# Kernel optimization log

Hardware: AMD Instinct MI355X
Metric: run time of the kernel (lower is better)

Reference implementation:

```python
import jax, jax.numpy as jnp
import numpy as np

H = 16          # num_attention_heads
D = 1024        # hidden_size
HD = D // H     # attention_head_size = 64


def setup_inputs() -> dict:
    key = jax.random.key(0)
    ks = jax.random.split(key, 9)
    s = 1.0 / np.sqrt(D)
    return {
        "hidden_states": jax.random.normal(ks[0], (4, 1024, D), jnp.float32),
        "encoder_hidden_states": jax.random.normal(ks[1], (4, 1024, D), jnp.float32),
        "attention_mask": jnp.zeros((4, 1, 1, 2048), jnp.float32),
        "Wq": jax.random.normal(ks[2], (D, D), jnp.float32) * s,
        "bq": jnp.zeros((D,), jnp.float32),
        "Wk": jax.random.normal(ks[3], (D, D), jnp.float32) * s,
        "bk": jnp.zeros((D,), jnp.float32),
        "Wv": jax.random.normal(ks[4], (D, D), jnp.float32) * s,
        "bv": jnp.zeros((D,), jnp.float32),
    }


def _split_heads(x):
    # [B, S, D] -> [B, H, S, HD]
    B, S, _ = x.shape
    return x.reshape(B, S, H, HD).transpose(0, 2, 1, 3)


def reference(hidden_states, encoder_hidden_states, attention_mask, Wq, bq, Wk, bk, Wv, bv):
    # KV over concat(encoder, decoder); Q over decoder hidden states only.
    all_hidden = jnp.concatenate([encoder_hidden_states, hidden_states], axis=1)  # [B, Skv, D]
    q = _split_heads(hidden_states @ Wq + bq)        # [B, H, Sq, HD]
    k = _split_heads(all_hidden @ Wk + bk)           # [B, H, Skv, HD]
    v = _split_heads(all_hidden @ Wv + bv)           # [B, H, Skv, HD]

    scores = jnp.einsum("bhqd,bhkd->bhqk", q, k) / np.sqrt(HD).astype(np.float32)
    scores = scores + attention_mask                 # additive mask, broadcast
    probs = jax.nn.softmax(scores, axis=-1)          # dropout p=0 (eval)
    ctx = jnp.einsum("bhqk,bhkd->bhqd", probs, v)    # [B, H, Sq, HD]
    B, _, Sq, _ = ctx.shape
    return ctx.transpose(0, 2, 1, 3).reshape(B, Sq, D)
```

## Files before the change

### kernel.cpp

```cpp
#include <hip/hip_runtime.h>


typedef _Float16 f16;
typedef __attribute__((ext_vector_type(4))) _Float16 half4;
typedef __attribute__((ext_vector_type(8))) _Float16 half8;
typedef __attribute__((ext_vector_type(4))) float floatx4;
typedef __attribute__((ext_vector_type(16))) float floatx16;
typedef __attribute__((ext_vector_type(4))) unsigned int uint4v;

__global__ void wt_kernel(const float* __restrict__ W, f16* __restrict__ Wt) {
    __shared__ float tile[32][33];
    int k0 = blockIdx.y * 32, n0 = blockIdx.x * 32;
    int tx = threadIdx.x, ty = threadIdx.y;
    #pragma unroll
    for (int i = 0; i < 32; i += 8)
        tile[ty + i][tx] = W[(k0 + ty + i) * 1024 + n0 + tx];
    __syncthreads();
    #pragma unroll
    for (int i = 0; i < 32; i += 8)
        Wt[(n0 + ty + i) * 1024 + k0 + tx] = (f16)tile[tx][ty + i];
}

__global__ void cvt_kernel(const float* __restrict__ hid, const float* __restrict__ enc,
                           f16* __restrict__ Aall) {
    int t = blockIdx.x * 256 + threadIdx.x;
    int rowg = t >> 7, col = (t & 127) * 8;
    int b = rowg >> 11, r = rowg & 2047;
    const float* src = (r < 1024 ? enc + ((size_t)b * 1024 + r) * 1024
                                 : hid + ((size_t)b * 1024 + (r - 1024)) * 1024) + col;
    float4 v0 = *(const float4*)src, v1 = *(const float4*)(src + 4);
    half8 o;
    o[0] = (f16)v0.x; o[1] = (f16)v0.y; o[2] = (f16)v0.z; o[3] = (f16)v0.w;
    o[4] = (f16)v1.x; o[5] = (f16)v1.y; o[6] = (f16)v1.z; o[7] = (f16)v1.w;
    *(half8*)(Aall + (size_t)rowg * 1024 + col) = o;
}

__launch_bounds__(256)
__global__ void qkv_gemm(const f16* __restrict__ Aall, const f16* __restrict__ Wt,
                         const float* __restrict__ bias, f16* __restrict__ out, int mode) {
    __shared__ f16 At[128 * 40];
    __shared__ f16 Bt[128 * 40];

    int tid = threadIdx.x;
    int m0 = blockIdx.x * 128, n0 = blockIdx.y * 128;
    int wid = tid >> 6, lane = tid & 63;
    int wm = (wid >> 1) * 64, wn = (wid & 1) * 64;
    int lr = lane & 15, lg = lane >> 4;

    floatx4 acc[4][4];
    #pragma unroll
    for (int i = 0; i < 4; i++)
        #pragma unroll
        for (int j = 0; j < 4; j++) acc[i][j] = (floatx4)(0.f);

    int tr2 = tid >> 2, tk2 = (tid & 3) * 8;
    const f16 *a0src, *a1src;
    {
        int mA0 = m0 + tr2, mA1 = mA0 + 64;
        if (mode == 0) {
            int b0 = mA0 >> 10, b1 = mA1 >> 10;
            a0src = Aall + ((size_t)(b0 * 2048 + 1024 + (mA0 & 1023))) * 1024 + tk2;
            a1src = Aall + ((size_t)(b1 * 2048 + 1024 + (mA1 & 1023))) * 1024 + tk2;
        } else {
            a0src = Aall + (size_t)mA0 * 1024 + tk2;
            a1src = Aall + (size_t)mA1 * 1024 + tk2;
        }
    }
    const f16* b0src = Wt + (size_t)(n0 + tr2) * 1024 + tk2;
    const f16* b1src = Wt + (size_t)(n0 + tr2 + 64) * 1024 + tk2;

    half8 ra0 = *(const half8*)a0src, ra1 = *(const half8*)a1src;
    half8 rb0 = *(const half8*)b0src, rb1 = *(const half8*)b1src;

    for (int k0 = 0; k0 < 1024; k0 += 32) {
        __syncthreads();
        *(half8*)&At[tr2 * 40 + tk2]        = ra0;
        *(half8*)&At[(tr2 + 64) * 40 + tk2] = ra1;
        *(half8*)&Bt[tr2 * 40 + tk2]        = rb0;
        *(half8*)&Bt[(tr2 + 64) * 40 + tk2] = rb1;
        __syncthreads();
        if (k0 < 992) {
            ra0 = *(const half8*)(a0src + k0 + 32);
            ra1 = *(const half8*)(a1src + k0 + 32);
            rb0 = *(const half8*)(b0src + k0 + 32);
            rb1 = *(const half8*)(b1src + k0 + 32);
        }

        half8 a[4], bf[4];
        #pragma unroll
        for (int i = 0; i < 4; i++)
            a[i] = *(const half8*)&At[(wm + i * 16 + lr) * 40 + lg * 8];
        #pragma unroll
        for (int j = 0; j < 4; j++)
            bf[j] = *(const half8*)&Bt[(wn + j * 16 + lr) * 40 + lg * 8];
        __builtin_amdgcn_s_setprio(1);
        #pragma unroll
        for (int i = 0; i < 4; i++)
            #pragma unroll
            for (int j = 0; j < 4; j++)
                acc[i][j] = __builtin_amdgcn_mfma_f32_16x16x32_f16(a[i], bf[j], acc[i][j], 0, 0, 0);
        __builtin_amdgcn_s_setprio(0);
    }

    if (mode == 2) {
        #pragma unroll
        for (int i = 0; i < 4; i++) {
            int mbase = m0 + wm + i * 16 + lg * 4;
            int b = mbase >> 11, s = mbase & 2047;
            #pragma unroll
            for (int j = 0; j < 4; j++) {
                int n = n0 + wn + j * 16 + lr;
                int h = n >> 6, d = n & 63;
                float bv = bias[n];
                half4 w;
                #pragma unroll
                for (int r = 0; r < 4; r++) w[r] = (f16)(acc[i][j][r] + bv);
                *(half4*)(out + ((size_t)((b * 16 + h) * 64 + d)) * 2048 + s) = w;
            }
        }
    } else {
        int Sout = (mode == 0) ? 1024 : 2048;
        #pragma unroll
        for (int i = 0; i < 4; i++) {
            int mbase = m0 + wm + i * 16 + lg * 4;
            #pragma unroll
            for (int j = 0; j < 4; j++) {
                int n = n0 + wn + j * 16 + lr;
                int h = n >> 6, d = n & 63;
                float bv = bias[n];
                #pragma unroll
                for (int r = 0; r < 4; r++) {
                    int m = mbase + r;
                    int b = (mode == 0) ? (m >> 10) : (m >> 11);
                    int s = (mode == 0) ? (m & 1023) : (m & 2047);
                    out[((size_t)(b * 16 + h) * Sout + s) * 64 + d] = (f16)(acc[i][j][r] + bv);
                }
            }
        }
    }
}

__device__ inline half8 pack_swap(float s0, float s1, float s2, float s3,
                                  float s4, float s5, float s6, float s7) {
    unsigned a0 = __builtin_bit_cast(unsigned, __builtin_amdgcn_cvt_pkrtz(s0, s1));
    unsigned b0 = __builtin_bit_cast(unsigned, __builtin_amdgcn_cvt_pkrtz(s4, s5));
    unsigned a1 = __builtin_bit_cast(unsigned, __builtin_amdgcn_cvt_pkrtz(s2, s3));
    unsigned b1 = __builtin_bit_cast(unsigned, __builtin_amdgcn_cvt_pkrtz(s6, s7));
    asm("v_permlane32_swap_b32 %0, %1" : "+v"(a0), "+v"(b0));
    asm("v_permlane32_swap_b32 %0, %1" : "+v"(a1), "+v"(b1));
    uint4v w = {a0, a1, b0, b1};
    return __builtin_bit_cast(half8, w);
}

__device__ inline half8 pack_noswap(float s0, float s1, float s2, float s3,
                                    float s4, float s5, float s6, float s7) {
    unsigned w0 = __builtin_bit_cast(unsigned, __builtin_amdgcn_cvt_pkrtz(s0, s1));
    unsigned w1 = __builtin_bit_cast(unsigned, __builtin_amdgcn_cvt_pkrtz(s2, s3));
    unsigned w2 = __builtin_bit_cast(unsigned, __builtin_amdgcn_cvt_pkrtz(s4, s5));
    unsigned w3 = __builtin_bit_cast(unsigned, __builtin_amdgcn_cvt_pkrtz(s6, s7));
    uint4v w = {w0, w1, w2, w3};
    return __builtin_bit_cast(half8, w);
}

__launch_bounds__(256)
__global__ void attn_kernel(const f16* __restrict__ Q, const f16* __restrict__ K,
                            const f16* __restrict__ Vt, const float* __restrict__ mask,
                            float* __restrict__ out) {
    __shared__ f16 Kt[64 * 72];
    __shared__ f16 Vtt[64 * 72];
    __shared__ float maskLds[2048];

    const float LOG2E = 1.4426950408889634f;
    int tid = threadIdx.x;
    int wid = tid >> 6, lane = tid & 63;
    int l31 = lane & 31, l5 = lane >> 5;
    int bh = blockIdx.y, b = bh >> 4, h = bh & 15;
    int q = blockIdx.x * 128 + wid * 32 + l31;

    half8 pa, pcode;
    #pragma unroll
    for (int j = 0; j < 8; j++) { pa[j] = (f16)0; pcode[j] = (f16)(8 * l5 + j); }
    if (l31 < 16 && (l31 >> 3) == l5) pa[l31 & 7] = (f16)1;
    floatx16 pd = __builtin_amdgcn_mfma_f32_32x32x16_f16(pa, pcode, (floatx16)0.f, 0, 0, 0);
    float r4 = __shfl(pd[0], 32);
    bool twoblk = (r4 > 6.0f);

    const float* maskp = mask + b * 2048;
    for (int i = tid; i < 512; i += 256) {
        float4 mv = ((const float4*)maskp)[i];
        mv.x *= LOG2E; mv.y *= LOG2E; mv.z *= LOG2E; mv.w *= LOG2E;
        ((float4*)maskLds)[i] = mv;
    }

    const f16* qrow = Q + ((size_t)bh * 1024 + q) * 64;
    half8 qf[4];
    if (!twoblk) {
        #pragma unroll
        for (int ks = 0; ks < 4; ks++)
            qf[ks] = *(const half8*)(qrow + ks * 16 + l5 * 8);
    } else {
        #pragma unroll
        for (int ks = 0; ks < 4; ks++) {
            half4 lo = *(const half4*)(qrow + ks * 16 + 4 * l5);
            half4 hi = *(const half4*)(qrow + ks * 16 + 8 + 4 * l5);
            qf[ks][0] = lo[0]; qf[ks][1] = lo[1]; qf[ks][2] = lo[2]; qf[ks][3] = lo[3];
            qf[ks][4] = hi[0]; qf[ks][5] = hi[1]; qf[ks][6] = hi[2]; qf[ks][7] = hi[3];
        }
    }
    const f16 qs = (f16)(0.125f * 1.4426950408889634f);
    #pragma unroll
    for (int ks = 0; ks < 4; ks++)
        #pragma unroll
        for (int x = 0; x < 8; x++) qf[ks][x] *= qs;

    floatx16 o0 = (floatx16)0.f, o1 = (floatx16)0.f;
    float m_run = -1e30f, l_run = 0.f;

    int sr = tid >> 2, sc = (tid & 3) * 16;
    const f16* Ksrc = K + ((size_t)bh * 2048 + sr) * 64 + sc;
    const f16* Vsrc = Vt + ((size_t)(bh * 64 + sr)) * 2048 + sc;

    half8 rk0 = *(const half8*)(Ksrc);
    half8 rk1 = *(const half8*)(Ksrc + 8);
    half8 rv0 = *(const half8*)(Vsrc);
    half8 rv1 = *(const half8*)(Vsrc + 8);

    for (int kv0 = 0; kv0 < 2048; kv0 += 64) {
        __syncthreads();
        *(half8*)&Kt[sr * 72 + sc]      = rk0;
        *(half8*)&Kt[sr * 72 + sc + 8]  = rk1;
        *(half8*)&Vtt[sr * 72 + sc]     = rv0;
        *(half8*)&Vtt[sr * 72 + sc + 8] = rv1;
        __syncthreads();
        if (kv0 < 2048 - 64) {
            rk0 = *(const half8*)(Ksrc + (size_t)(kv0 + 64) * 64);
            rk1 = *(const half8*)(Ksrc + (size_t)(kv0 + 64) * 64 + 8);
            rv0 = *(const half8*)(Vsrc + kv0 + 64);
            rv1 = *(const half8*)(Vsrc + kv0 + 64 + 8);
        }

        floatx16 sf0, sf1;
        #pragma unroll
        for (int g = 0; g < 4; g++) {
            float4 mk0 = *(const float4*)&maskLds[kv0 + 8 * g + 4 * l5];
            float4 mk1 = *(const float4*)&maskLds[kv0 + 32 + 8 * g + 4 * l5];
            #pragma unroll
            for (int i = 0; i < 4; i++) {
                sf0[4 * g + i] = ((const float*)&mk0)[i];
                sf1[4 * g + i] = ((const float*)&mk1)[i];
            }
        }

        __builtin_amdgcn_s_setprio(1);
        #pragma unroll
        for (int ks = 0; ks < 4; ks++) {
            half8 k0 = *(const half8*)&Kt[l31 * 72 + ks * 16 + l5 * 8];
            half8 k1 = *(const half8*)&Kt[(32 + l31) * 72 + ks * 16 + l5 * 8];
            sf0 = __builtin_amdgcn_mfma_f32_32x32x16_f16(k0, qf[ks], sf0, 0, 0, 0);
            sf1 = __builtin_amdgcn_mfma_f32_32x32x16_f16(k1, qf[ks], sf1, 0, 0, 0);
        }
        __builtin_amdgcn_s_setprio(0);

        float pmax = -1e30f;
        #pragma unroll
        for (int r = 0; r < 16; r++)
            pmax = fmaxf(pmax, fmaxf(sf0[r], sf1[r]));

        if (!__all(pmax - m_run <= 8.0f)) {
            float rmax = fmaxf(pmax, __shfl_xor(pmax, 32));
            float mnew = fmaxf(m_run, rmax);
            float alpha = exp2f(m_run - mnew);
            l_run *= alpha;
            #pragma unroll
            for (int r = 0; r < 16; r++) { o0[r] *= alpha; o1[r] *= alpha; }
            m_run = mnew;
        }

        float ls = 0.f;
        #pragma unroll
        for (int r = 0; r < 16; r++) {
            float p0 = exp2f(sf0[r] - m_run);
            float p1 = exp2f(sf1[r] - m_run);
            sf0[r] = p0; sf1[r] = p1;
            ls += p0 + p1;
        }
        ls += __shfl_xor(ls, 32);
        l_run += ls;

        half8 pb[4];
        if (!twoblk) {
            pb[0] = pack_swap(sf0[0], sf0[1], sf0[2], sf0[3], sf0[4], sf0[5], sf0[6], sf0[7]);
            pb[1] = pack_swap(sf0[8], sf0[9], sf0[10], sf0[11], sf0[12], sf0[13], sf0[14], sf0[15]);
            pb[2] = pack_swap(sf1[0], sf1[1], sf1[2], sf1[3], sf1[4], sf1[5], sf1[6], sf1[7]);
            pb[3] = pack_swap(sf1[8], sf1[9], sf1[10], sf1[11], sf1[12], sf1[13], sf1[14], sf1[15]);
        } else {
            pb[0] = pack_noswap(sf0[0], sf0[1], sf0[2], sf0[3], sf0[4], sf0[5], sf0[6], sf0[7]);
            pb[1] = pack_noswap(sf0[8], sf0[9], sf0[10], sf0[11], sf0[12], sf0[13], sf0[14], sf0[15]);
            pb[2] = pack_noswap(sf1[0], sf1[1], sf1[2], sf1[3], sf1[4], sf1[5], sf1[6], sf1[7]);
            pb[3] = pack_noswap(sf1[8], sf1[9], sf1[10], sf1[11], sf1[12], sf1[13], sf1[14], sf1[15]);
        }

        __builtin_amdgcn_s_setprio(1);
        #pragma unroll
        for (int kb = 0; kb < 4; kb++) {
            half8 v0 = *(const half8*)&Vtt[l31 * 72 + kb * 16 + l5 * 8];
            half8 v1 = *(const half8*)&Vtt[(32 + l31) * 72 + kb * 16 + l5 * 8];
            o0 = __builtin_amdgcn_mfma_f32_32x32x16_f16(v0, pb[kb], o0, 0, 0, 0);
            o1 = __builtin_amdgcn_mfma_f32_32x32x16_f16(v1, pb[kb], o1, 0, 0, 0);
        }
        __builtin_amdgcn_s_setprio(0);
    }

    float inv = 1.f / l_run;
    float* orow = out + ((size_t)(b * 1024 + q)) * 1024 + h * 64;
    #pragma unroll
    for (int g = 0; g < 4; g++) {
        float4 r0 = {o0[4 * g] * inv, o0[4 * g + 1] * inv, o0[4 * g + 2] * inv, o0[4 * g + 3] * inv};
        float4 r1 = {o1[4 * g] * inv, o1[4 * g + 1] * inv, o1[4 * g + 2] * inv, o1[4 * g + 3] * inv};
        *(float4*)&orow[8 * g + 4 * l5]      = r0;
        *(float4*)&orow[32 + 8 * g + 4 * l5] = r1;
    }
}

extern "C" void kernel_launch(void* const* d_in, const int* in_sizes, int n_in,
                              void* d_out, int out_size, void* d_ws, size_t ws_size,
                              hipStream_t stream) {
    const float* hid  = (const float*)d_in[0];
    const float* enc  = (const float*)d_in[1];
    const float* mask = (const float*)d_in[2];
    const float* Wq   = (const float*)d_in[3];
    const float* bq   = (const float*)d_in[4];
    const float* Wk   = (const float*)d_in[5];
    const float* bk   = (const float*)d_in[6];
    const float* Wv   = (const float*)d_in[7];
    const float* bv   = (const float*)d_in[8];
    float* out = (float*)d_out;

    char* ws = (char*)d_ws;
    f16* Wtq  = (f16*)(ws + ((size_t)0 << 20));
    f16* Wtk  = (f16*)(ws + ((size_t)2 << 20));
    f16* Wtv  = (f16*)(ws + ((size_t)4 << 20));
    f16* Aall = (f16*)(ws + ((size_t)6 << 20));
    f16* Qw   = (f16*)(ws + ((size_t)22 << 20));
    f16* Kw   = (f16*)(ws + ((size_t)30 << 20));
    f16* Vtw  = (f16*)(ws + ((size_t)46 << 20));

    dim3 tb(32, 8);
    wt_kernel<<<dim3(32, 32), tb, 0, stream>>>(Wq, Wtq);
    wt_kernel<<<dim3(32, 32), tb, 0, stream>>>(Wk, Wtk);
    wt_kernel<<<dim3(32, 32), tb, 0, stream>>>(Wv, Wtv);
    cvt_kernel<<<4096, 256, 0, stream>>>(hid, enc, Aall);

    qkv_gemm<<<dim3(32, 8), 256, 0, stream>>>(Aall, Wtq, bq, Qw, 0);
    qkv_gemm<<<dim3(64, 8), 256, 0, stream>>>(Aall, Wtk, bk, Kw, 1);
    qkv_gemm<<<dim3(64, 8), 256, 0, stream>>>(Aall, Wtv, bv, Vtw, 2);

    attn_kernel<<<dim3(8, 64), 256, 0, stream>>>(Qw, Kw, Vtw, mask, out);
}
```

Before: 168.9 us.

## Split attention KV range across two blocks and merge partial outputs

Splits the 2048-key attention into two halves handled by separate blocks (grid z=2), each writing unnormalized fp16 partial outputs plus running max and sum. A new merge kernel combines the two partials with log-sum-exp rescaling and writes the fp32 output. The aim is to double the number of attention blocks (512 to 1024) for better occupancy across the CUs. In exchange it adds an extra kernel launch, extra global traffic for the partials, and fp16 rounding of the unnormalized accumulators. The partial buffers reuse workspace regions that earlier held the transposed weights and the converted activations, which are dead by that point.

Result: slower. 180.9 us (+7.1%).

```diff
diff --git a/kernel.cpp b/kernel.cpp
--- a/kernel.cpp
+++ b/kernel.cpp
@@ -7,6 +7,8 @@
 typedef __attribute__((ext_vector_type(4))) float floatx4;
 typedef __attribute__((ext_vector_type(16))) float floatx16;
 typedef __attribute__((ext_vector_type(4))) unsigned int uint4v;
+
+#define OPSTRIDE ((size_t)4194304)
 
 __global__ void wt_kernel(const float* __restrict__ W, f16* __restrict__ Wt) {
     __shared__ float tile[32][33];
@@ -165,16 +167,17 @@
 __launch_bounds__(256)
 __global__ void attn_kernel(const f16* __restrict__ Q, const f16* __restrict__ K,
                             const f16* __restrict__ Vt, const float* __restrict__ mask,
-                            float* __restrict__ out) {
+                            f16* __restrict__ Opart, float* __restrict__ mlbuf) {
     __shared__ f16 Kt[64 * 72];
     __shared__ f16 Vtt[64 * 72];
-    __shared__ float maskLds[2048];
+    __shared__ float maskLds[1024];
 
     const float LOG2E = 1.4426950408889634f;
     int tid = threadIdx.x;
     int wid = tid >> 6, lane = tid & 63;
     int l31 = lane & 31, l5 = lane >> 5;
-    int bh = blockIdx.y, b = bh >> 4, h = bh & 15;
+    int bh = blockIdx.y, b = bh >> 4;
+    int sp = blockIdx.z;
     int q = blockIdx.x * 128 + wid * 32 + l31;
 
     half8 pa, pcode;
@@ -185,11 +188,10 @@
     float r4 = __shfl(pd[0], 32);
     bool twoblk = (r4 > 6.0f);
 
-    const float* maskp = mask + b * 2048;
-    for (int i = tid; i < 512; i += 256) {
-        float4 mv = ((const float4*)maskp)[i];
+    {
+        float4 mv = ((const float4*)(mask + b * 2048 + sp * 1024))[tid];
         mv.x *= LOG2E; mv.y *= LOG2E; mv.z *= LOG2E; mv.w *= LOG2E;
-        ((float4*)maskLds)[i] = mv;
+        ((float4*)maskLds)[tid] = mv;
     }
 
     const f16* qrow = Q + ((size_t)bh * 1024 + q) * 64;
@@ -217,22 +219,22 @@
     float m_run = -1e30f, l_run = 0.f;
 
     int sr = tid >> 2, sc = (tid & 3) * 16;
-    const f16* Ksrc = K + ((size_t)bh * 2048 + sr) * 64 + sc;
-    const f16* Vsrc = Vt + ((size_t)(bh * 64 + sr)) * 2048 + sc;
+    const f16* Ksrc = K + ((size_t)bh * 2048 + sp * 1024 + sr) * 64 + sc;
+    const f16* Vsrc = Vt + ((size_t)(bh * 64 + sr)) * 2048 + sp * 1024 + sc;
 
     half8 rk0 = *(const half8*)(Ksrc);
     half8 rk1 = *(const half8*)(Ksrc + 8);
     half8 rv0 = *(const half8*)(Vsrc);
     half8 rv1 = *(const half8*)(Vsrc + 8);
 
-    for (int kv0 = 0; kv0 < 2048; kv0 += 64) {
+    for (int kv0 = 0; kv0 < 1024; kv0 += 64) {
         __syncthreads();
         *(half8*)&Kt[sr * 72 + sc]      = rk0;
         *(half8*)&Kt[sr * 72 + sc + 8]  = rk1;
         *(half8*)&Vtt[sr * 72 + sc]     = rv0;
         *(half8*)&Vtt[sr * 72 + sc + 8] = rv1;
         __syncthreads();
-        if (kv0 < 2048 - 64) {
+        if (kv0 < 1024 - 64) {
             rk0 = *(const half8*)(Ksrc + (size_t)(kv0 + 64) * 64);
             rk1 = *(const half8*)(Ksrc + (size_t)(kv0 + 64) * 64 + 8);
             rv0 = *(const half8*)(Vsrc + kv0 + 64);
@@ -311,15 +313,45 @@
         __builtin_amdgcn_s_setprio(0);
     }
 
-    float inv = 1.f / l_run;
-    float* orow = out + ((size_t)(b * 1024 + q)) * 1024 + h * 64;
+    size_t row = (size_t)bh * 1024 + q;
+    size_t obase = (size_t)sp * OPSTRIDE + row * 64;
     #pragma unroll
     for (int g = 0; g < 4; g++) {
-        float4 r0 = {o0[4 * g] * inv, o0[4 * g + 1] * inv, o0[4 * g + 2] * inv, o0[4 * g + 3] * inv};
-        float4 r1 = {o1[4 * g] * inv, o1[4 * g + 1] * inv, o1[4 * g + 2] * inv, o1[4 * g + 3] * inv};
-        *(float4*)&orow[8 * g + 4 * l5]      = r0;
-        *(float4*)&orow[32 + 8 * g + 4 * l5] = r1;
-    }
+        half4 w0, w1;
+        #pragma unroll
+        for (int r = 0; r < 4; r++) {
+            w0[r] = (f16)o0[4 * g + r];
+            w1[r] = (f16)o1[4 * g + r];
+        }
+        *(half4*)(Opart + obase + 8 * g + 4 * l5)      = w0;
+        *(half4*)(Opart + obase + 32 + 8 * g + 4 * l5) = w1;
+    }
+    if (l5 == 0) {
+        float2 v = {m_run, l_run};
+        *(float2*)(mlbuf + ((size_t)sp * 65536 + row) * 2) = v;
+    }
+}
+
+__global__ void merge_kernel(const f16* __restrict__ Op, const float* __restrict__ ml,
+                             float* __restrict__ out) {
+    int t = blockIdx.x * 256 + threadIdx.x;
+    int row = t >> 3, dc = (t & 7) * 8;
+    int bh = row >> 10, q = row & 1023, b = bh >> 4, h = bh & 15;
+    float2 ml0 = *(const float2*)(ml + (size_t)row * 2);
+    float2 ml1 = *(const float2*)(ml + ((size_t)65536 + row) * 2);
+    float mm = fmaxf(ml0.x, ml1.x);
+    float w0 = exp2f(ml0.x - mm), w1 = exp2f(ml1.x - mm);
+    float inv = 1.f / (ml0.y * w0 + ml1.y * w1);
+    w0 *= inv; w1 *= inv;
+    half8 a = *(const half8*)(Op + (size_t)row * 64 + dc);
+    half8 c = *(const half8*)(Op + OPSTRIDE + (size_t)row * 64 + dc);
+    float* orow = out + ((size_t)(b * 1024 + q)) * 1024 + h * 64 + dc;
+    float4 lo = {(float)a[0] * w0 + (float)c[0] * w1, (float)a[1] * w0 + (float)c[1] * w1,
+                 (float)a[2] * w0 + (float)c[2] * w1, (float)a[3] * w0 + (float)c[3] * w1};
+    float4 hi = {(float)a[4] * w0 + (float)c[4] * w1, (float)a[5] * w0 + (float)c[5] * w1,
+                 (float)a[6] * w0 + (float)c[6] * w1, (float)a[7] * w0 + (float)c[7] * w1};
+    *(float4*)orow = lo;
+    *(float4*)(orow + 4) = hi;
 }
 
 extern "C" void kernel_launch(void* const* d_in, const int* in_sizes, int n_in,
@@ -344,6 +376,8 @@
     f16* Qw   = (f16*)(ws + ((size_t)22 << 20));
     f16* Kw   = (f16*)(ws + ((size_t)30 << 20));
     f16* Vtw  = (f16*)(ws + ((size_t)46 << 20));
+    f16*   Opart = (f16*)(ws + ((size_t)0 << 20));
+    float* mlbuf = (float*)(ws + ((size_t)17 << 20));
 
     dim3 tb(32, 8);
     wt_kernel<<<dim3(32, 32), tb, 0, stream>>>(Wq, Wtq);
@@ -355,5 +389,6 @@
     qkv_gemm<<<dim3(64, 8), 256, 0, stream>>>(Aall, Wtk, bk, Kw, 1);
     qkv_gemm<<<dim3(64, 8), 256, 0, stream>>>(Aall, Wtv, bv, Vtw, 2);
 
-    attn_kernel<<<dim3(8, 64), 256, 0, stream>>>(Qw, Kw, Vtw, mask, out);
-}
+    attn_kernel<<<dim3(8, 64, 2), 256, 0, stream>>>(Qw, Kw, Vtw, mask, Opart, mlbuf);
+    merge_kernel<<<2048, 256, 0, stream>>>(Opart, mlbuf, out);
+}
```
